# Performance work log

Hardware: AMD Instinct MI355X
Metric: run time of the kernel (lower is better)

Reference implementation:

```python
import jax, jax.numpy as jnp
import numpy as np

B, FEAT, SPD_H, CTRL_H, N_CMD = 32768, 512, 128, 256, 4


def _p(key, shape, fan_in):
    # torch nn.Linear default init: U(-1/sqrt(fan_in), 1/sqrt(fan_in))
    lim = 1.0 / np.sqrt(fan_in)
    return jax.random.uniform(key, shape, jnp.float32, -lim, lim)


def setup_inputs() -> dict:
    key = jax.random.key(0)
    ks = iter(jax.random.split(key, 32))
    inp = {
        "feat": jax.random.normal(next(ks), (B, FEAT), jnp.float32),
        "speed": jax.random.uniform(next(ks), (B,), jnp.float32),
        "command": jax.random.randint(next(ks), (B,), 0, N_CMD, jnp.int32),
        "ms_w1": _p(next(ks), (1, SPD_H), 1), "ms_b1": _p(next(ks), (SPD_H,), 1),
        "ms_w2": _p(next(ks), (SPD_H, SPD_H), SPD_H), "ms_b2": _p(next(ks), (SPD_H,), SPD_H),
        "ms_w3": _p(next(ks), (SPD_H, SPD_H), SPD_H), "ms_b3": _p(next(ks), (SPD_H,), SPD_H),
        # speed_pred_module: 512 -> 256 -> 256 -> 1
        "sp_w1": _p(next(ks), (FEAT, CTRL_H), FEAT), "sp_b1": _p(next(ks), (CTRL_H,), FEAT),
        "sp_w2": _p(next(ks), (CTRL_H, CTRL_H), CTRL_H), "sp_b2": _p(next(ks), (CTRL_H,), CTRL_H),
        "sp_w3": _p(next(ks), (CTRL_H, 1), CTRL_H), "sp_b3": _p(next(ks), (1,), CTRL_H),
        # join_module: Linear(640, 512)
        "join_w": _p(next(ks), (FEAT + SPD_H, FEAT), FEAT + SPD_H),
        "join_b": _p(next(ks), (FEAT,), FEAT + SPD_H),
        # 4 control heads: 512 -> 256 -> 256 -> 3 (stacked on expert axis e)
        "ctrl_w1": _p(next(ks), (N_CMD, FEAT, CTRL_H), FEAT), "ctrl_b1": _p(next(ks), (N_CMD, CTRL_H), FEAT),
        "ctrl_w2": _p(next(ks), (N_CMD, CTRL_H, CTRL_H), CTRL_H), "ctrl_b2": _p(next(ks), (N_CMD, CTRL_H), CTRL_H),
        "ctrl_w3": _p(next(ks), (N_CMD, CTRL_H, 3), CTRL_H), "ctrl_b3": _p(next(ks), (N_CMD, 3), CTRL_H),
    }
    return inp


def _mlp(x, w1, b1, w2, b2, w3, b3):
    # FullyConnectedNet: Linear, ReLU, Linear, Dropout(p=0 -> noop), ReLU, Linear
    h = jax.nn.relu(x @ w1 + b1)
    h = jax.nn.relu(h @ w2 + b2)
    return h @ w3 + b3


def reference(feat, speed, command,
              ms_w1, ms_b1, ms_w2, ms_b2, ms_w3, ms_b3,
              sp_w1, sp_b1, sp_w2, sp_b2, sp_w3, sp_b3,
              join_w, join_b,
              ctrl_w1, ctrl_b1, ctrl_w2, ctrl_b2, ctrl_w3, ctrl_b3):
    v = _mlp(speed[:, None], ms_w1, ms_b1, ms_w2, ms_b2, ms_w3, ms_b3)      # [B,128]
    joined = jnp.concatenate([feat, v], axis=1) @ join_w + join_b           # [B,512]
    v_p = _mlp(feat, sp_w1, sp_b1, sp_w2, sp_b2, sp_w3, sp_b3)              # [B,1]
    # command-indexed dispatch: compute all 4 heads densely, then select per sample
    h1 = jax.nn.relu(jnp.einsum('bd,edh->beh', joined, ctrl_w1) + ctrl_b1)  # [B,4,256]
    h2 = jax.nn.relu(jnp.einsum('beh,ehk->bek', h1, ctrl_w2) + ctrl_b2)     # [B,4,256]
    act_all = jnp.einsum('bek,eko->beo', h2, ctrl_w3) + ctrl_b3             # [B,4,3]
    action = jnp.take_along_axis(act_all, command[:, None, None].astype(jnp.int32), axis=1)[:, 0]  # [B,3]
    throttle = jax.nn.sigmoid(action[:, 0])
    steering = jnp.tanh(action[:, 1])
    brake = jax.nn.sigmoid(action[:, 2])
    return v_p, throttle, brake, steering
```

## Files before the change

kernel.cpp:

```cpp
#include <hip/hip_runtime.h>
#include <hip/hip_bf16.h>
#include <stdint.h>
#include <math.h>

#define BB 32768
#define FEAT 512
#define SPD_H 128
#define CTRL_H 256
#define NCMD 4

typedef __attribute__((ext_vector_type(8))) short bf16x8;
typedef __attribute__((ext_vector_type(4))) float f32x4;

__device__ __forceinline__ unsigned short f2bf(float f) {
  union { float f; uint32_t u; } v; v.f = f;
  uint32_t u = v.u;
  return (unsigned short)((u + 0x7fffu + ((u >> 16) & 1u)) >> 16);
}

__device__ __forceinline__ void async16(const unsigned short* g, unsigned short* l) {
  __builtin_amdgcn_global_load_lds(
      (const __attribute__((address_space(1))) unsigned int*)g,
      (__attribute__((address_space(3))) unsigned int*)l, 16, 0, 0);
}

__device__ __forceinline__ void gemm128(
    const unsigned short* __restrict__ A, int lda,
    const int* __restrict__ perm, int m_start, int m_cnt,
    const unsigned short* __restrict__ W, const float* __restrict__ bi,
    unsigned short* __restrict__ C, int ldc, int relu, int K, int mt, int nt) {
  extern __shared__ __align__(16) unsigned char dynsm[];
  unsigned short* As = (unsigned short*)dynsm;
  unsigned short* Bs = As + 128 * 32;

  const int m0 = mt * 128;
  if (m0 >= m_cnt) return;
  const int n0 = nt * 128;
  const int t = threadIdx.x;
  const int w = t >> 6, lane = t & 63;
  const int wm = w & 1, wn = w >> 1;

  f32x4 acc[4][4];
#pragma unroll
  for (int i = 0; i < 4; ++i)
#pragma unroll
    for (int j = 0; j < 4; ++j)
#pragma unroll
      for (int r = 0; r < 4; ++r) acc[i][j][r] = 0.f;

  const int fr = lane & 15;
  const int fk = (lane >> 4) * 8;

  const unsigned short* agp[2]; const unsigned short* bgp[2];
  unsigned short* al[2]; unsigned short* bl[2];
#pragma unroll
  for (int it = 0; it < 2; ++it) {
    int row = w * 32 + it * 16 + (lane >> 2);
    int seg8 = (lane & 3) * 8;
    int rl = m0 + row;
    if (rl >= m_cnt) rl = m_cnt - 1;
    int grow = perm ? perm[m_start + rl] : (m_start + rl);
    agp[it] = A + (size_t)grow * lda + seg8;
    bgp[it] = W + (size_t)(n0 + row) * K + seg8;
    al[it] = As + (w * 32 + it * 16) * 32;
    bl[it] = Bs + (w * 32 + it * 16) * 32;
  }

  for (int k0 = 0; k0 < K; k0 += 32) {
#pragma unroll
    for (int it = 0; it < 2; ++it) {
      async16(agp[it] + k0, al[it]);
      async16(bgp[it] + k0, bl[it]);
    }
    __syncthreads();
    bf16x8 af[4], bfv[4];
#pragma unroll
    for (int i = 0; i < 4; ++i)
      af[i] = *(const bf16x8*)(As + (wm * 64 + i * 16 + fr) * 32 + fk);
#pragma unroll
    for (int j = 0; j < 4; ++j)
      bfv[j] = *(const bf16x8*)(Bs + (wn * 64 + j * 16 + fr) * 32 + fk);
#pragma unroll
    for (int i = 0; i < 4; ++i)
#pragma unroll
      for (int j = 0; j < 4; ++j)
        acc[i][j] = __builtin_amdgcn_mfma_f32_16x16x32_bf16(af[i], bfv[j], acc[i][j], 0, 0, 0);
    __syncthreads();
  }

  const int rquad = (lane >> 4) * 4;
  const int cidx = lane & 15;

  float bv[4];
#pragma unroll
  for (int j = 0; j < 4; ++j) bv[j] = bi ? bi[n0 + wn * 64 + j * 16 + cidx] : 0.f;

  unsigned short (*bscr)[136] = (unsigned short(*)[136])dynsm;
#pragma unroll
  for (int c = 0; c < 4; ++c) {
    if (wm == (c >> 1)) {
#pragma unroll
      for (int j = 0; j < 4; ++j) {
#pragma unroll
        for (int ii = 0; ii < 2; ++ii) {
          int i = 2 * (c & 1) + ii;
          int lr = ii * 16 + rquad;
#pragma unroll
          for (int r = 0; r < 4; ++r) {
            float v = acc[i][j][r] + bv[j];
            if (relu) v = fmaxf(v, 0.f);
            bscr[lr + r][wn * 64 + j * 16 + cidx] = f2bf(v);
          }
        }
      }
    }
    __syncthreads();
#pragma unroll
    for (int q = 0; q < 2; ++q) {
      int sg = t + 256 * q;
      int lr = sg >> 4, cs = (sg & 15) * 8;
      int grow = m0 + c * 32 + lr;
      if (grow < m_cnt)
        *(bf16x8*)(C + (size_t)(m_start + grow) * ldc + (n0 + cs)) =
            *(const bf16x8*)(&bscr[lr][cs]);
    }
    __syncthreads();
  }
}

struct WSeg { const float* src; unsigned short* dst; int K; int N; int ldd; };
struct PrepArgs {
  WSeg s[12];
  int start[13];
  const float* join_w; unsigned short* wjbf;
  const float* feat; unsigned short* ajoin;
  const int* cmd; int* wavecnt;
  const float* join_b; const float* ctrl_w1; const float* ctrl_b1; float* b_f;
};
__launch_bounds__(256)
__global__ void k_prep(PrepArgs a) {
  int bx = blockIdx.x, t = threadIdx.x;
  if (bx < 16384) {
    int idx = bx * 256 + t;
    int i = idx >> 7;
    int j4 = (idx & 127) << 2;
    float4 f = *(const float4*)(a.feat + (size_t)i * FEAT + j4);
    ushort4 o;
    o.x = f2bf(f.x); o.y = f2bf(f.y); o.z = f2bf(f.z); o.w = f2bf(f.w);
    *(ushort4*)(a.ajoin + (size_t)i * 640 + j4) = o;
    return;
  }
  int rel = bx - 16384;
  if (rel < 320) {
    int idx = rel * 256 + t;
    float4 f = *(const float4*)(a.join_w + (size_t)idx * 4);
    ushort4 o;
    o.x = f2bf(f.x); o.y = f2bf(f.y); o.z = f2bf(f.z); o.w = f2bf(f.w);
    *(ushort4*)(a.wjbf + (size_t)idx * 4) = o;
    return;
  }
  rel -= 320;
  if (rel < a.start[12]) {
    __shared__ float tb[32][33];
    int si = 0;
    while (rel >= a.start[si + 1]) ++si;
    WSeg sg = a.s[si];
    int tile = rel - a.start[si];
    int tkx = sg.K >> 5;
    int tn = tile / tkx;
    int tk = tile - tn * tkx;
    int k0 = tk * 32, n0 = tn * 32;
    int tx = t & 31, ty = t >> 5;
#pragma unroll
    for (int j = 0; j < 4; ++j)
      tb[ty + j * 8][tx] = sg.src[(size_t)(k0 + ty + j * 8) * sg.N + n0 + tx];
    __syncthreads();
#pragma unroll
    for (int j = 0; j < 4; ++j)
      sg.dst[(size_t)(n0 + ty + j * 8) * sg.ldd + k0 + tx] = f2bf(tb[tx][ty + j * 8]);
    return;
  }
  rel -= a.start[12];
  if (rel < 128) {
    int i = rel * 256 + t;
    int c = a.cmd[i];
    int wid = i >> 6;
    int lane = t & 63;
#pragma unroll
    for (int cv = 0; cv < NCMD; ++cv) {
      unsigned long long m = __ballot(c == cv);
      if (lane == 0) a.wavecnt[cv * 512 + wid] = __popcll(m);
    }
    return;
  }
  int e = rel - 128;
  float s0 = a.ctrl_b1[e * 256 + t], s1 = 0.f, s2 = 0.f, s3 = 0.f;
  const float* w = a.ctrl_w1 + (size_t)e * 512 * 256 + t;
#pragma unroll 4
  for (int m = 0; m < 512; m += 4) {
    s0 = fmaf(a.join_b[m + 0], w[(size_t)(m + 0) * 256], s0);
    s1 = fmaf(a.join_b[m + 1], w[(size_t)(m + 1) * 256], s1);
    s2 = fmaf(a.join_b[m + 2], w[(size_t)(m + 2) * 256], s2);
    s3 = fmaf(a.join_b[m + 3], w[(size_t)(m + 3) * 256], s3);
  }
  a.b_f[e * 256 + t] = (s0 + s1) + (s2 + s3);
}

struct MidArgs {
  const int* cmd; const int* wavecnt; int* perm; int* offs;
  const unsigned short* c_w1t; const unsigned short* wjbf; unsigned short* wf_t;
  const float* speed;
  const float* ms_w1; const float* ms_b1;
  const unsigned short* ms_w2t; const float* ms_b2;
  const unsigned short* ms_w3t; const float* ms_b3;
  unsigned short* ajoin;
  int* tile_e; int* tile_r0; int* ntl;
};
__launch_bounds__(256)
__global__ void k_mid(MidArgs a) {
  int b = blockIdx.x, t = threadIdx.x;
  if (b >= 168) {
    extern __shared__ __align__(16) unsigned char dynsm[];
    unsigned short (*hw)[136] = (unsigned short(*)[136])dynsm;
    unsigned short* BsM = (unsigned short*)(dynsm + 128 * 136 * 2);
    const int m0 = (b - 168) * 128;
    const int w = t >> 6, lane = t & 63;
    const int wm = w & 1, wn = w >> 1;
    const int fr = lane & 15, fk = (lane >> 4) * 8;
    const int rquad = (lane >> 4) * 4, cidx = lane & 15;
    {
      int r = t >> 1, half = t & 1;
      float s = a.speed[m0 + r];
#pragma unroll
      for (int c0 = 0; c0 < 64; c0 += 4) {
        int c = half * 64 + c0;
        float4 wv = *(const float4*)(a.ms_w1 + c);
        float4 bv = *(const float4*)(a.ms_b1 + c);
        hw[r][c + 0] = f2bf(fmaxf(fmaf(s, wv.x, bv.x), 0.f));
        hw[r][c + 1] = f2bf(fmaxf(fmaf(s, wv.y, bv.y), 0.f));
        hw[r][c + 2] = f2bf(fmaxf(fmaf(s, wv.z, bv.z), 0.f));
        hw[r][c + 3] = f2bf(fmaxf(fmaf(s, wv.w, bv.w), 0.f));
      }
    }
    __syncthreads();
    for (int layer = 0; layer < 2; ++layer) {
      const unsigned short* Wt = layer ? a.ms_w3t : a.ms_w2t;
      const float* bb = layer ? a.ms_b3 : a.ms_b2;
      f32x4 acc[4][4];
#pragma unroll
      for (int i = 0; i < 4; ++i)
#pragma unroll
        for (int j = 0; j < 4; ++j)
#pragma unroll
          for (int r = 0; r < 4; ++r) acc[i][j][r] = 0.f;
      for (int k0 = 0; k0 < 128; k0 += 32) {
#pragma unroll
        for (int it = 0; it < 2; ++it) {
          int row = w * 32 + it * 16 + (lane >> 2);
          async16(Wt + (size_t)row * 128 + k0 + (lane & 3) * 8,
                  BsM + (w * 32 + it * 16) * 32);
        }
        __syncthreads();
        bf16x8 af[4], bfv[4];
#pragma unroll
        for (int i = 0; i < 4; ++i)
          af[i] = *(const bf16x8*)(&hw[wm * 64 + i * 16 + fr][k0 + fk]);
#pragma unroll
        for (int j = 0; j < 4; ++j)
          bfv[j] = *(const bf16x8*)(BsM + (wn * 64 + j * 16 + fr) * 32 + fk);
#pragma unroll
        for (int i = 0; i < 4; ++i)
#pragma unroll
          for (int j = 0; j < 4; ++j)
            acc[i][j] = __builtin_amdgcn_mfma_f32_16x16x32_bf16(af[i], bfv[j], acc[i][j], 0, 0, 0);
        __syncthreads();
      }
#pragma unroll
      for (int j = 0; j < 4; ++j) {
        int col = wn * 64 + j * 16 + cidx;
        float bv = bb[col];
#pragma unroll
        for (int i = 0; i < 4; ++i) {
          int row = wm * 64 + i * 16 + rquad;
#pragma unroll
          for (int r = 0; r < 4; ++r) {
            float v = acc[i][j][r] + bv;
            if (layer == 0) v = fmaxf(v, 0.f);
            hw[row + r][col] = f2bf(v);
          }
        }
      }
      __syncthreads();
    }
    {
      int r = t >> 1, half = t & 1;
#pragma unroll
      for (int c8 = 0; c8 < 8; ++c8)
        *(bf16x8*)(a.ajoin + (size_t)(m0 + r) * 640 + 512 + half * 64 + c8 * 8) =
            *(const bf16x8*)(&hw[r][half * 64 + c8 * 8]);
    }
    return;
  }
  if (b >= 128) {
    int idx = b - 128;
    int mt = idx & 7, nt = idx >> 3;
    gemm128(a.c_w1t, 512, nullptr, 0, 1024, a.wjbf, nullptr, a.wf_t, 640, 0, 512, mt, nt);
    return;
  }
  __shared__ int pf[NCMD][4];
  __shared__ int tot[NCMD];
  int c = t >> 6, lane = t & 63;
  int v[8]; int s = 0;
#pragma unroll
  for (int q = 0; q < 8; ++q) { v[q] = a.wavecnt[c * 512 + lane * 8 + q]; s += v[q]; }
  int p = s;
#pragma unroll
  for (int m = 1; m < 64; m <<= 1) { int o = __shfl_up(p, m, 64); if (lane >= m) p += o; }
  int excl = p - s;
  if (lane == 63) tot[c] = p;
  if (lane == ((4 * b) >> 3)) {
    int base_off = (4 * b) & 7;
    int run = excl;
#pragma unroll
    for (int q = 0; q < 8; ++q) {
      if (q >= base_off && q < base_off + 4) pf[c][q - base_off] = run;
      run += v[q];
    }
  }
  __syncthreads();
  int soffs[NCMD + 1];
  soffs[0] = 0;
#pragma unroll
  for (int e = 0; e < NCMD; ++e) soffs[e + 1] = soffs[e] + tot[e];
  if (b == 0 && t == 0)
    for (int e = 0; e <= NCMD; ++e) a.offs[e] = soffs[e];
  int i = b * 256 + t;
  int mc = a.cmd[i];
  int lwid = t >> 6;
  int rank = 0, base = 0;
#pragma unroll
  for (int cv = 0; cv < NCMD; ++cv) {
    unsigned long long m = __ballot(mc == cv);
    if (mc == cv) {
      rank = __popcll(m & ((1ull << lane) - 1ull));
      base = soffs[cv] + pf[cv][lwid];
    }
  }
  a.perm[base + rank] = i;

  if (b == 0) {
    int toff[NCMD + 1];
    toff[0] = 0;
#pragma unroll
    for (int ee = 0; ee < NCMD; ++ee) toff[ee + 1] = toff[ee] + ((tot[ee] + 63) >> 6);
    if (t == 0) a.ntl[0] = toff[NCMD];
    for (int ti = t; ti < toff[NCMD]; ti += 256) {
      int ee = 0;
      while (ti >= toff[ee + 1]) ++ee;
      a.tile_e[ti] = ee;
      a.tile_r0[ti] = soffs[ee] + (ti - toff[ee]) * 64;
    }
  }
}

struct TailArgs {
  const unsigned short* ajoin;
  const unsigned short* wf_t;  const float* b_f;
  const unsigned short* sp_w1t; const float* sp_b1;
  const unsigned short* c_w2t; const float* ctrl_b2;
  const unsigned short* sp_w2t; const float* sp_b2;
  const float* ctrl_w3; const float* ctrl_b3;
  const float* sp_w3; const float* sp_b3;
  const int* perm; const int* seg;
  const int* tile_e; const int* tile_r0; const int* ntl;
  float* out;
};
__launch_bounds__(256, 3)
__global__ void k_tail(TailArgs a) {
  extern __shared__ __align__(16) unsigned char dynsm[];
  unsigned short* As = (unsigned short*)dynsm;
  unsigned short* h1 = (unsigned short*)(dynsm + 16384);
  float* pscr = (float*)dynsm;

  const int t = threadIdx.x;
  const int w = t >> 6, lane = t & 63;
  const int fr = lane & 15, fcg = lane >> 4;
  const int rquad = fcg * 4, cidx = fr;
  const int fkS = ((fcg ^ (fr & 3)) << 3);

  int is_sp, e = 0, NC;
  const unsigned short *W1, *W2;
  const float *b1, *b2;
  int r0, rend;
  if (blockIdx.x < 512) {
    is_sp = 1; NC = 8;
    W1 = a.sp_w1t; W2 = a.sp_w2t; b1 = a.sp_b1; b2 = a.sp_b2;
    r0 = blockIdx.x * 64; rend = BB;
  } else {
    int ti = blockIdx.x - 512;
    if (ti >= a.ntl[0]) return;
    is_sp = 0; e = a.tile_e[ti]; NC = 10;
    W1 = a.wf_t + (size_t)e * 256 * 640;
    W2 = a.c_w2t + (size_t)e * 65536;
    b1 = a.b_f + e * 256; b2 = a.ctrl_b2 + e * 256;
    r0 = a.tile_r0[ti]; rend = a.seg[e + 1];
  }
  const int K = is_sp ? 512 : 640;

  const unsigned short* agp[2];
  {
    int rl = r0 + w * 16 + (lane >> 2);
    if (rl >= rend) rl = rend - 1;
    int grow = is_sp ? rl : a.perm[rl];
    const unsigned short* g0 =
        a.ajoin + (size_t)grow * 640 + (((lane & 3) ^ ((lane >> 2) & 3)) << 3);
    agp[0] = g0; agp[1] = g0 + 32;
  }
  unsigned short* alb0 = As + w * 16 * 32;
  unsigned short* alb1 = As + 2048 + w * 16 * 32;

  const unsigned short* bp[4];
#pragma unroll
  for (int j = 0; j < 4; ++j)
    bp[j] = W1 + (size_t)(w * 64 + j * 16 + fr) * K + fcg * 8;

  f32x4 acc[4][4];
#pragma unroll
  for (int i = 0; i < 4; ++i)
#pragma unroll
    for (int j = 0; j < 4; ++j)
#pragma unroll
      for (int r = 0; r < 4; ++r) acc[i][j][r] = 0.f;

  async16(agp[0], alb0);
  async16(agp[1], alb1);

  for (int c = 0; c < NC; ++c) {
    const int cur = (c & 1) * 4096;
    if (c + 1 < NC) {
      const int nb = ((c + 1) & 1) * 4096;
      async16(agp[0] + (c + 1) * 64, alb0 + nb);
      async16(agp[1] + (c + 1) * 64, alb1 + nb);
      asm volatile("s_waitcnt vmcnt(2)" ::: "memory");
    } else {
      asm volatile("s_waitcnt vmcnt(0)" ::: "memory");
    }
    __builtin_amdgcn_s_barrier();
#pragma unroll
    for (int ks = 0; ks < 2; ++ks) {
      const int k0 = c * 64 + ks * 32;
      bf16x8 af[4], bv[4];
#pragma unroll
      for (int i = 0; i < 4; ++i)
        af[i] = *(const bf16x8*)(As + cur + ks * 2048 + (i * 16 + fr) * 32 + fkS);
#pragma unroll
      for (int j = 0; j < 4; ++j)
        bv[j] = *(const bf16x8*)(bp[j] + k0);
#pragma unroll
      for (int i = 0; i < 4; ++i)
#pragma unroll
        for (int j = 0; j < 4; ++j)
          acc[i][j] = __builtin_amdgcn_mfma_f32_16x16x32_bf16(af[i], bv[j], acc[i][j], 0, 0, 0);
    }
    __builtin_amdgcn_s_barrier();
  }

#pragma unroll
  for (int j = 0; j < 4; ++j) {
    const int col = w * 64 + j * 16 + cidx;
    const float bj = b1[col];
    const int c8 = col >> 3, cl = col & 7;
#pragma unroll
    for (int i = 0; i < 4; ++i) {
#pragma unroll
      for (int r = 0; r < 4; ++r) {
        const int row = i * 16 + rquad + r;
        h1[(row << 8) + (((c8 ^ (row & 7)) << 3) | cl)] =
            f2bf(fmaxf(acc[i][j][r] + bj, 0.f));
      }
    }
  }
  __syncthreads();

  const unsigned short* bp2[4];
#pragma unroll
  for (int j = 0; j < 4; ++j)
    bp2[j] = W2 + (size_t)(w * 64 + j * 16 + fr) * 256 + fcg * 8;

#pragma unroll
  for (int i = 0; i < 4; ++i)
#pragma unroll
    for (int j = 0; j < 4; ++j)
#pragma unroll
      for (int r = 0; r < 4; ++r) acc[i][j][r] = 0.f;

#pragma unroll 2
  for (int k0 = 0; k0 < 256; k0 += 32) {
    bf16x8 af[4], bv[4];
#pragma unroll
    for (int i = 0; i < 4; ++i) {
      const int row = i * 16 + fr;
      const int c8 = (k0 >> 3) + fcg;
      af[i] = *(const bf16x8*)(h1 + (row << 8) + ((c8 ^ (row & 7)) << 3));
    }
#pragma unroll
    for (int j = 0; j < 4; ++j)
      bv[j] = *(const bf16x8*)(bp2[j] + k0);
#pragma unroll
    for (int i = 0; i < 4; ++i)
#pragma unroll
      for (int j = 0; j < 4; ++j)
        acc[i][j] = __builtin_amdgcn_mfma_f32_16x16x32_bf16(af[i], bv[j], acc[i][j], 0, 0, 0);
  }

  float b2v[4], w30[4], w31[4], w32[4];
#pragma unroll
  for (int j = 0; j < 4; ++j) {
    const int col = w * 64 + j * 16 + cidx;
    b2v[j] = b2[col];
    if (is_sp) {
      w30[j] = a.sp_w3[col]; w31[j] = 0.f; w32[j] = 0.f;
    } else {
      const float* wp = a.ctrl_w3 + (size_t)e * 768 + col * 3;
      w30[j] = wp[0]; w31[j] = wp[1]; w32[j] = wp[2];
    }
  }
#pragma unroll
  for (int i = 0; i < 4; ++i) {
#pragma unroll
    for (int r = 0; r < 4; ++r) {
      float s0 = 0.f, s1 = 0.f, s2 = 0.f;
#pragma unroll
      for (int j = 0; j < 4; ++j) {
        const float v = fmaxf(acc[i][j][r] + b2v[j], 0.f);
        s0 = fmaf(v, w30[j], s0);
        if (!is_sp) { s1 = fmaf(v, w31[j], s1); s2 = fmaf(v, w32[j], s2); }
      }
#pragma unroll
      for (int m = 1; m <= 8; m <<= 1) {
        s0 += __shfl_xor(s0, m, 64);
        if (!is_sp) { s1 += __shfl_xor(s1, m, 64); s2 += __shfl_xor(s2, m, 64); }
      }
      if (cidx == 0) {
        const int row = i * 16 + rquad + r;
        pscr[(row * 4 + w) * 3 + 0] = s0;
        if (!is_sp) {
          pscr[(row * 4 + w) * 3 + 1] = s1;
          pscr[(row * 4 + w) * 3 + 2] = s2;
        }
      }
    }
  }
  __syncthreads();

  if (is_sp) {
    if (t < 64) {
      float s = pscr[t * 12] + pscr[t * 12 + 3] + pscr[t * 12 + 6] + pscr[t * 12 + 9]
              + a.sp_b3[0];
      a.out[r0 + t] = s;
    }
  } else {
    if (t < 192) {
      const int row = t / 3, o = t - row * 3;
      const int rl = r0 + row;
      if (rl < rend) {
        float s = pscr[row * 12 + o] + pscr[row * 12 + 3 + o] +
                  pscr[row * 12 + 6 + o] + pscr[row * 12 + 9 + o] +
                  a.ctrl_b3[e * 3 + o];
        const int orig = a.perm[rl];
        if (o == 0)      a.out[BB + orig]     = 1.f / (1.f + __expf(-s));
        else if (o == 2) a.out[2 * BB + orig] = 1.f / (1.f + __expf(-s));
        else             a.out[3 * BB + orig] = tanhf(s);
      }
    }
  }
}

static inline size_t align256(size_t x) { return (x + 255) & ~(size_t)255; }

extern "C" void kernel_launch(void* const* d_in, const int* in_sizes, int n_in,
                              void* d_out, int out_size, void* d_ws, size_t ws_size,
                              hipStream_t stream) {
  const float* feat   = (const float*)d_in[0];
  const float* speed  = (const float*)d_in[1];
  const int*   command= (const int*)d_in[2];
  const float* ms_w1  = (const float*)d_in[3];
  const float* ms_b1  = (const float*)d_in[4];
  const float* ms_w2  = (const float*)d_in[5];
  const float* ms_b2  = (const float*)d_in[6];
  const float* ms_w3  = (const float*)d_in[7];
  const float* ms_b3  = (const float*)d_in[8];
  const float* sp_w1  = (const float*)d_in[9];
  const float* sp_b1  = (const float*)d_in[10];
  const float* sp_w2  = (const float*)d_in[11];
  const float* sp_b2  = (const float*)d_in[12];
  const float* sp_w3  = (const float*)d_in[13];
  const float* sp_b3  = (const float*)d_in[14];
  const float* join_w = (const float*)d_in[15];
  const float* join_b = (const float*)d_in[16];
  const float* ctrl_w1= (const float*)d_in[17];
  const float* ctrl_b1= (const float*)d_in[18];
  const float* ctrl_w2= (const float*)d_in[19];
  const float* ctrl_b2= (const float*)d_in[20];
  const float* ctrl_w3= (const float*)d_in[21];
  const float* ctrl_b3= (const float*)d_in[22];
  float* out = (float*)d_out;

  char* ws = (char*)d_ws;
  size_t off = 0;
  auto alloc = [&](size_t bytes) -> char* { char* p = ws + off; off = align256(off + bytes); return p; };

  unsigned short* ajoin  = (unsigned short*)alloc((size_t)BB * 640 * 2);
  unsigned short* wtp    = (unsigned short*)alloc(1998848ull * 2);
  int* perm    = (int*)alloc((size_t)BB * 4);
  int* cnt     = (int*)alloc(64);
  int* wavecnt = (int*)alloc(4 * 512 * 4);
  float* b_f   = (float*)alloc(4 * 256 * 4);
  int* tile_e  = (int*)alloc(520 * 4);
  int* tile_r0 = (int*)alloc(520 * 4);
  int* ntl     = (int*)alloc(64);

  unsigned short* sp_w1t = wtp;
  unsigned short* sp_w2t = wtp + 131072;
  unsigned short* ms_w2t = wtp + 196608;
  unsigned short* ms_w3t = wtp + 212992;
  unsigned short* c_w1t  = wtp + 229376;
  unsigned short* c_w2t  = wtp + 753664;
  unsigned short* wjbf   = wtp + 1015808;
  unsigned short* wf_t   = wtp + 1343488;

  PrepArgs P;
  P.s[0] = { sp_w1, sp_w1t, 512, 256, 512 };
  P.s[1] = { sp_w2, sp_w2t, 256, 256, 256 };
  P.s[2] = { ms_w2, ms_w2t, 128, 128, 128 };
  P.s[3] = { ms_w3, ms_w3t, 128, 128, 128 };
  for (int e = 0; e < 4; ++e) P.s[4 + e] = { ctrl_w1 + (size_t)e * 512 * 256, c_w1t + (size_t)e * 131072, 512, 256, 512 };
  for (int e = 0; e < 4; ++e) P.s[8 + e] = { ctrl_w2 + (size_t)e * 256 * 256, c_w2t + (size_t)e * 65536, 256, 256, 256 };
  P.start[0] = 0;
  for (int i = 0; i < 12; ++i)
    P.start[i + 1] = P.start[i] + (P.s[i].K >> 5) * (P.s[i].N >> 5);
  P.join_w = join_w; P.wjbf = wjbf;
  P.feat = feat; P.ajoin = ajoin;
  P.cmd = command; P.wavecnt = wavecnt;
  P.join_b = join_b; P.ctrl_w1 = ctrl_w1; P.ctrl_b1 = ctrl_b1; P.b_f = b_f;
  int prep_blocks = 16384 + 320 + P.start[12] + 128 + 4;

  k_prep<<<prep_blocks, 256, 0, stream>>>(P);

  MidArgs Mi;
  Mi.cmd = command; Mi.wavecnt = wavecnt; Mi.perm = perm; Mi.offs = cnt + 4;
  Mi.c_w1t = c_w1t; Mi.wjbf = wjbf; Mi.wf_t = wf_t;
  Mi.speed = speed;
  Mi.ms_w1 = ms_w1; Mi.ms_b1 = ms_b1;
  Mi.ms_w2t = ms_w2t; Mi.ms_b2 = ms_b2;
  Mi.ms_w3t = ms_w3t; Mi.ms_b3 = ms_b3;
  Mi.ajoin = ajoin;
  Mi.tile_e = tile_e; Mi.tile_r0 = tile_r0; Mi.ntl = ntl;
  k_mid<<<168 + 256, 256, 128 * 136 * 2 + 128 * 32 * 2, stream>>>(Mi);

  TailArgs T;
  T.ajoin = ajoin; T.wf_t = wf_t; T.b_f = b_f;
  T.sp_w1t = sp_w1t; T.sp_b1 = sp_b1;
  T.c_w2t = c_w2t; T.ctrl_b2 = ctrl_b2;
  T.sp_w2t = sp_w2t; T.sp_b2 = sp_b2;
  T.ctrl_w3 = ctrl_w3; T.ctrl_b3 = ctrl_b3;
  T.sp_w3 = sp_w3; T.sp_b3 = sp_b3;
  T.perm = perm; T.seg = cnt + 4;
  T.tile_e = tile_e; T.tile_r0 = tile_r0; T.ntl = ntl;
  T.out = out;
  k_tail<<<dim3(512 + 516), 256, 49152, stream>>>(T);
}
```

Measured before the change: 240.7 us.

## Fuse feat bf16 conversion into tail GEMM loads and halve row tiles

Removes the separate pass that converts feat to bf16 into a 640-wide joined buffer. The tail kernel now reads fp32 feat directly, packs it to bf16 in registers, and writes it into a swizzled LDS tile. The speed-MLP output goes to its own 128-wide buffer instead of the joined one. Row tiles shrink from 64 to 32, which doubles the block count and raises the occupancy hint to 4. In exchange, async global-to-LDS loads become register staging with two barriers per K-chunk, and weight reads are amortized over fewer rows.

Measured after the change: 267.8 us. 1.11x slower.

```diff
diff --git a/kernel.cpp b/kernel.cpp
--- a/kernel.cpp
+++ b/kernel.cpp
@@ -16,6 +16,15 @@
   union { float f; uint32_t u; } v; v.f = f;
   uint32_t u = v.u;
   return (unsigned short)((u + 0x7fffu + ((u >> 16) & 1u)) >> 16);
+}
+
+__device__ __forceinline__ bf16x8 pack8(float4 a, float4 b) {
+  bf16x8 r;
+  r[0] = (short)f2bf(a.x); r[1] = (short)f2bf(a.y);
+  r[2] = (short)f2bf(a.z); r[3] = (short)f2bf(a.w);
+  r[4] = (short)f2bf(b.x); r[5] = (short)f2bf(b.y);
+  r[6] = (short)f2bf(b.z); r[7] = (short)f2bf(b.w);
+  return r;
 }
 
 __device__ __forceinline__ void async16(const unsigned short* g, unsigned short* l) {
@@ -133,33 +142,21 @@
   WSeg s[12];
   int start[13];
   const float* join_w; unsigned short* wjbf;
-  const float* feat; unsigned short* ajoin;
   const int* cmd; int* wavecnt;
   const float* join_b; const float* ctrl_w1; const float* ctrl_b1; float* b_f;
 };
 __launch_bounds__(256)
 __global__ void k_prep(PrepArgs a) {
   int bx = blockIdx.x, t = threadIdx.x;
-  if (bx < 16384) {
+  if (bx < 320) {
     int idx = bx * 256 + t;
-    int i = idx >> 7;
-    int j4 = (idx & 127) << 2;
-    float4 f = *(const float4*)(a.feat + (size_t)i * FEAT + j4);
-    ushort4 o;
-    o.x = f2bf(f.x); o.y = f2bf(f.y); o.z = f2bf(f.z); o.w = f2bf(f.w);
-    *(ushort4*)(a.ajoin + (size_t)i * 640 + j4) = o;
-    return;
-  }
-  int rel = bx - 16384;
-  if (rel < 320) {
-    int idx = rel * 256 + t;
     float4 f = *(const float4*)(a.join_w + (size_t)idx * 4);
     ushort4 o;
     o.x = f2bf(f.x); o.y = f2bf(f.y); o.z = f2bf(f.z); o.w = f2bf(f.w);
     *(ushort4*)(a.wjbf + (size_t)idx * 4) = o;
     return;
   }
-  rel -= 320;
+  int rel = bx - 320;
   if (rel < a.start[12]) {
     __shared__ float tb[32][33];
     int si = 0;
@@ -213,7 +210,7 @@
   const float* ms_w1; const float* ms_b1;
   const unsigned short* ms_w2t; const float* ms_b2;
   const unsigned short* ms_w3t; const float* ms_b3;
-  unsigned short* ajoin;
+  unsigned short* msout;
   int* tile_e; int* tile_r0; int* ntl;
 };
 __launch_bounds__(256)
@@ -296,7 +293,7 @@
       int r = t >> 1, half = t & 1;
 #pragma unroll
       for (int c8 = 0; c8 < 8; ++c8)
-        *(bf16x8*)(a.ajoin + (size_t)(m0 + r) * 640 + 512 + half * 64 + c8 * 8) =
+        *(bf16x8*)(a.msout + (size_t)(m0 + r) * 128 + half * 64 + c8 * 8) =
             *(const bf16x8*)(&hw[r][half * 64 + c8 * 8]);
     }
     return;
@@ -352,19 +349,20 @@
     int toff[NCMD + 1];
     toff[0] = 0;
 #pragma unroll
-    for (int ee = 0; ee < NCMD; ++ee) toff[ee + 1] = toff[ee] + ((tot[ee] + 63) >> 6);
+    for (int ee = 0; ee < NCMD; ++ee) toff[ee + 1] = toff[ee] + ((tot[ee] + 31) >> 5);
     if (t == 0) a.ntl[0] = toff[NCMD];
     for (int ti = t; ti < toff[NCMD]; ti += 256) {
       int ee = 0;
       while (ti >= toff[ee + 1]) ++ee;
       a.tile_e[ti] = ee;
-      a.tile_r0[ti] = soffs[ee] + (ti - toff[ee]) * 64;
+      a.tile_r0[ti] = soffs[ee] + (ti - toff[ee]) * 32;
     }
   }
 }
 
 struct TailArgs {
-  const unsigned short* ajoin;
+  const float* feat;
+  const unsigned short* msout;
   const unsigned short* wf_t;  const float* b_f;
   const unsigned short* sp_w1t; const float* sp_b1;
   const unsigned short* c_w2t; const float* ctrl_b2;
@@ -375,29 +373,29 @@
   const int* tile_e; const int* tile_r0; const int* ntl;
   float* out;
 };
-__launch_bounds__(256, 3)
+__launch_bounds__(256, 4)
 __global__ void k_tail(TailArgs a) {
   extern __shared__ __align__(16) unsigned char dynsm[];
   unsigned short* As = (unsigned short*)dynsm;
-  unsigned short* h1 = (unsigned short*)(dynsm + 16384);
+  unsigned short* h1 = (unsigned short*)(dynsm + 8192);
   float* pscr = (float*)dynsm;
 
   const int t = threadIdx.x;
   const int w = t >> 6, lane = t & 63;
   const int fr = lane & 15, fcg = lane >> 4;
   const int rquad = fcg * 4, cidx = fr;
-  const int fkS = ((fcg ^ (fr & 3)) << 3);
+  const int row_s = t >> 3, cg = t & 7;
 
   int is_sp, e = 0, NC;
   const unsigned short *W1, *W2;
   const float *b1, *b2;
   int r0, rend;
-  if (blockIdx.x < 512) {
+  if (blockIdx.x < 1024) {
     is_sp = 1; NC = 8;
     W1 = a.sp_w1t; W2 = a.sp_w2t; b1 = a.sp_b1; b2 = a.sp_b2;
-    r0 = blockIdx.x * 64; rend = BB;
+    r0 = blockIdx.x * 32; rend = BB;
   } else {
-    int ti = blockIdx.x - 512;
+    int ti = blockIdx.x - 1024;
     if (ti >= a.ntl[0]) return;
     is_sp = 0; e = a.tile_e[ti]; NC = 10;
     W1 = a.wf_t + (size_t)e * 256 * 640;
@@ -407,62 +405,74 @@
   }
   const int K = is_sp ? 512 : 640;
 
-  const unsigned short* agp[2];
+  const float* fsrc; const unsigned short* msrc;
   {
-    int rl = r0 + w * 16 + (lane >> 2);
+    int rl = r0 + row_s;
     if (rl >= rend) rl = rend - 1;
     int grow = is_sp ? rl : a.perm[rl];
-    const unsigned short* g0 =
-        a.ajoin + (size_t)grow * 640 + (((lane & 3) ^ ((lane >> 2) & 3)) << 3);
-    agp[0] = g0; agp[1] = g0 + 32;
-  }
-  unsigned short* alb0 = As + w * 16 * 32;
-  unsigned short* alb1 = As + 2048 + w * 16 * 32;
+    fsrc = a.feat + (size_t)grow * 512 + cg * 8;
+    msrc = a.msout + (size_t)grow * 128 + cg * 8;
+  }
+  unsigned short* wslot = As + row_s * 64 + ((cg ^ (row_s & 7)) << 3);
 
   const unsigned short* bp[4];
 #pragma unroll
   for (int j = 0; j < 4; ++j)
     bp[j] = W1 + (size_t)(w * 64 + j * 16 + fr) * K + fcg * 8;
 
-  f32x4 acc[4][4];
-#pragma unroll
-  for (int i = 0; i < 4; ++i)
+  f32x4 acc[2][4];
+#pragma unroll
+  for (int i = 0; i < 2; ++i)
 #pragma unroll
     for (int j = 0; j < 4; ++j)
 #pragma unroll
       for (int r = 0; r < 4; ++r) acc[i][j][r] = 0.f;
 
-  async16(agp[0], alb0);
-  async16(agp[1], alb1);
+  {
+    float4 fa = *(const float4*)(fsrc);
+    float4 fb = *(const float4*)(fsrc + 4);
+    *(bf16x8*)(wslot) = pack8(fa, fb);
+  }
+  __syncthreads();
 
   for (int c = 0; c < NC; ++c) {
-    const int cur = (c & 1) * 4096;
-    if (c + 1 < NC) {
-      const int nb = ((c + 1) & 1) * 4096;
-      async16(agp[0] + (c + 1) * 64, alb0 + nb);
-      async16(agp[1] + (c + 1) * 64, alb1 + nb);
-      asm volatile("s_waitcnt vmcnt(2)" ::: "memory");
-    } else {
-      asm volatile("s_waitcnt vmcnt(0)" ::: "memory");
-    }
-    __builtin_amdgcn_s_barrier();
+    float4 fa, fb; bf16x8 mreg;
+    const int k0n = (c + 1) * 64;
+    const bool pre = (c + 1 < NC);
+    if (pre) {
+      if (k0n < 512) {
+        fa = *(const float4*)(fsrc + k0n);
+        fb = *(const float4*)(fsrc + k0n + 4);
+      } else {
+        mreg = *(const bf16x8*)(msrc + (k0n - 512));
+      }
+    }
+    const unsigned short* cbuf = As + (c & 1) * 2048;
 #pragma unroll
     for (int ks = 0; ks < 2; ++ks) {
       const int k0 = c * 64 + ks * 32;
-      bf16x8 af[4], bv[4];
-#pragma unroll
-      for (int i = 0; i < 4; ++i)
-        af[i] = *(const bf16x8*)(As + cur + ks * 2048 + (i * 16 + fr) * 32 + fkS);
+      bf16x8 af[2], bv[4];
+#pragma unroll
+      for (int i = 0; i < 2; ++i)
+        af[i] = *(const bf16x8*)(cbuf + (i * 16 + fr) * 64 +
+                                 (((ks * 4 + fcg) ^ (fr & 7)) << 3));
 #pragma unroll
       for (int j = 0; j < 4; ++j)
         bv[j] = *(const bf16x8*)(bp[j] + k0);
 #pragma unroll
-      for (int i = 0; i < 4; ++i)
+      for (int i = 0; i < 2; ++i)
 #pragma unroll
         for (int j = 0; j < 4; ++j)
           acc[i][j] = __builtin_amdgcn_mfma_f32_16x16x32_bf16(af[i], bv[j], acc[i][j], 0, 0, 0);
     }
-    __builtin_amdgcn_s_barrier();
+    __syncthreads();
+    if (pre) {
+      bf16x8 pk;
+      if (k0n < 512) pk = pack8(fa, fb);
+      else pk = mreg;
+      *(bf16x8*)(wslot + ((c + 1) & 1) * 2048) = pk;
+    }
+    __syncthreads();
   }
 
 #pragma unroll
@@ -471,7 +481,7 @@
     const float bj = b1[col];
     const int c8 = col >> 3, cl = col & 7;
 #pragma unroll
-    for (int i = 0; i < 4; ++i) {
+    for (int i = 0; i < 2; ++i) {
 #pragma unroll
       for (int r = 0; r < 4; ++r) {
         const int row = i * 16 + rquad + r;
@@ -488,7 +498,7 @@
     bp2[j] = W2 + (size_t)(w * 64 + j * 16 + fr) * 256 + fcg * 8;
 
 #pragma unroll
-  for (int i = 0; i < 4; ++i)
+  for (int i = 0; i < 2; ++i)
 #pragma unroll
     for (int j = 0; j < 4; ++j)
 #pragma unroll
@@ -496,9 +506,9 @@
 
 #pragma unroll 2
   for (int k0 = 0; k0 < 256; k0 += 32) {
-    bf16x8 af[4], bv[4];
-#pragma unroll
-    for (int i = 0; i < 4; ++i) {
+    bf16x8 af[2], bv[4];
+#pragma unroll
+    for (int i = 0; i < 2; ++i) {
       const int row = i * 16 + fr;
       const int c8 = (k0 >> 3) + fcg;
       af[i] = *(const bf16x8*)(h1 + (row << 8) + ((c8 ^ (row & 7)) << 3));
@@ -507,7 +517,7 @@
     for (int j = 0; j < 4; ++j)
       bv[j] = *(const bf16x8*)(bp2[j] + k0);
 #pragma unroll
-    for (int i = 0; i < 4; ++i)
+    for (int i = 0; i < 2; ++i)
 #pragma unroll
       for (int j = 0; j < 4; ++j)
         acc[i][j] = __builtin_amdgcn_mfma_f32_16x16x32_bf16(af[i], bv[j], acc[i][j], 0, 0, 0);
@@ -526,7 +536,7 @@
     }
   }
 #pragma unroll
-  for (int i = 0; i < 4; ++i) {
+  for (int i = 0; i < 2; ++i) {
 #pragma unroll
     for (int r = 0; r < 4; ++r) {
       float s0 = 0.f, s1 = 0.f, s2 = 0.f;
@@ -554,13 +564,13 @@
   __syncthreads();
 
   if (is_sp) {
-    if (t < 64) {
+    if (t < 32) {
       float s = pscr[t * 12] + pscr[t * 12 + 3] + pscr[t * 12 + 6] + pscr[t * 12 + 9]
               + a.sp_b3[0];
       a.out[r0 + t] = s;
     }
   } else {
-    if (t < 192) {
+    if (t < 96) {
       const int row = t / 3, o = t - row * 3;
       const int rl = r0 + row;
       if (rl < rend) {
@@ -610,14 +620,14 @@
   size_t off = 0;
   auto alloc = [&](size_t bytes) -> char* { char* p = ws + off; off = align256(off + bytes); return p; };
 
-  unsigned short* ajoin  = (unsigned short*)alloc((size_t)BB * 640 * 2);
+  unsigned short* msout  = (unsigned short*)alloc((size_t)BB * 128 * 2);
   unsigned short* wtp    = (unsigned short*)alloc(1998848ull * 2);
   int* perm    = (int*)alloc((size_t)BB * 4);
   int* cnt     = (int*)alloc(64);
   int* wavecnt = (int*)alloc(4 * 512 * 4);
   float* b_f   = (float*)alloc(4 * 256 * 4);
-  int* tile_e  = (int*)alloc(520 * 4);
-  int* tile_r0 = (int*)alloc(520 * 4);
+  int* tile_e  = (int*)alloc(1056 * 4);
+  int* tile_r0 = (int*)alloc(1056 * 4);
   int* ntl     = (int*)alloc(64);
 
   unsigned short* sp_w1t = wtp;
@@ -640,10 +650,9 @@
   for (int i = 0; i < 12; ++i)
     P.start[i + 1] = P.start[i] + (P.s[i].K >> 5) * (P.s[i].N >> 5);
   P.join_w = join_w; P.wjbf = wjbf;
-  P.feat = feat; P.ajoin = ajoin;
   P.cmd = command; P.wavecnt = wavecnt;
   P.join_b = join_b; P.ctrl_w1 = ctrl_w1; P.ctrl_b1 = ctrl_b1; P.b_f = b_f;
-  int prep_blocks = 16384 + 320 + P.start[12] + 128 + 4;
+  int prep_blocks = 320 + P.start[12] + 128 + 4;
 
   k_prep<<<prep_blocks, 256, 0, stream>>>(P);
 
@@ -654,12 +663,13 @@
   Mi.ms_w1 = ms_w1; Mi.ms_b1 = ms_b1;
   Mi.ms_w2t = ms_w2t; Mi.ms_b2 = ms_b2;
   Mi.ms_w3t = ms_w3t; Mi.ms_b3 = ms_b3;
-  Mi.ajoin = ajoin;
+  Mi.msout = msout;
   Mi.tile_e = tile_e; Mi.tile_r0 = tile_r0; Mi.ntl = ntl;
   k_mid<<<168 + 256, 256, 128 * 136 * 2 + 128 * 32 * 2, stream>>>(Mi);
 
   TailArgs T;
-  T.ajoin = ajoin; T.wf_t = wf_t; T.b_f = b_f;
+  T.feat = feat; T.msout = msout;
+  T.wf_t = wf_t; T.b_f = b_f;
   T.sp_w1t = sp_w1t; T.sp_b1 = sp_b1;
   T.c_w2t = c_w2t; T.ctrl_b2 = ctrl_b2;
   T.sp_w2t = sp_w2t; T.sp_b2 = sp_b2;
@@ -668,5 +678,5 @@
   T.perm = perm; T.seg = cnt + 4;
   T.tile_e = tile_e; T.tile_r0 = tile_r0; T.ntl = ntl;
   T.out = out;
-  k_tail<<<dim3(512 + 516), 256, 49152, stream>>>(T);
-}
+  k_tail<<<dim3(1024 + 1028), 256, 24576, stream>>>(T);
+}
```

## Fuse feat fp32-to-bf16 conversion into tail GEMM A-tile loads

Applied to the files above, without the earlier changes.

Drops the separate prep pass that converted feat to bf16 into a 640-wide joined buffer. The tail kernel now reads fp32 feat rows directly (through perm for the expert heads), converts them to bf16 in registers, and writes a swizzled 64-wide K tile into LDS. The speed-MLP output goes to its own narrow bf16 buffer. The async global-to-LDS copies become register-staged double buffering. This removes the large write and re-read of the intermediate, but the tail now reads twice as many bytes for feat and uses more registers. The expert heads and the speed-prediction path each re-read feat, so feat is fetched in fp32 more than once.

Result: faster. 230.0 us (-4.5%).

```diff
diff --git a/kernel.cpp b/kernel.cpp
--- a/kernel.cpp
+++ b/kernel.cpp
@@ -16,6 +16,15 @@
   union { float f; uint32_t u; } v; v.f = f;
   uint32_t u = v.u;
   return (unsigned short)((u + 0x7fffu + ((u >> 16) & 1u)) >> 16);
+}
+
+__device__ __forceinline__ bf16x8 pack8(float4 a, float4 b) {
+  bf16x8 r;
+  r[0] = (short)f2bf(a.x); r[1] = (short)f2bf(a.y);
+  r[2] = (short)f2bf(a.z); r[3] = (short)f2bf(a.w);
+  r[4] = (short)f2bf(b.x); r[5] = (short)f2bf(b.y);
+  r[6] = (short)f2bf(b.z); r[7] = (short)f2bf(b.w);
+  return r;
 }
 
 __device__ __forceinline__ void async16(const unsigned short* g, unsigned short* l) {
@@ -133,33 +142,21 @@
   WSeg s[12];
   int start[13];
   const float* join_w; unsigned short* wjbf;
-  const float* feat; unsigned short* ajoin;
   const int* cmd; int* wavecnt;
   const float* join_b; const float* ctrl_w1; const float* ctrl_b1; float* b_f;
 };
 __launch_bounds__(256)
 __global__ void k_prep(PrepArgs a) {
   int bx = blockIdx.x, t = threadIdx.x;
-  if (bx < 16384) {
+  if (bx < 320) {
     int idx = bx * 256 + t;
-    int i = idx >> 7;
-    int j4 = (idx & 127) << 2;
-    float4 f = *(const float4*)(a.feat + (size_t)i * FEAT + j4);
-    ushort4 o;
-    o.x = f2bf(f.x); o.y = f2bf(f.y); o.z = f2bf(f.z); o.w = f2bf(f.w);
-    *(ushort4*)(a.ajoin + (size_t)i * 640 + j4) = o;
-    return;
-  }
-  int rel = bx - 16384;
-  if (rel < 320) {
-    int idx = rel * 256 + t;
     float4 f = *(const float4*)(a.join_w + (size_t)idx * 4);
     ushort4 o;
     o.x = f2bf(f.x); o.y = f2bf(f.y); o.z = f2bf(f.z); o.w = f2bf(f.w);
     *(ushort4*)(a.wjbf + (size_t)idx * 4) = o;
     return;
   }
-  rel -= 320;
+  int rel = bx - 320;
   if (rel < a.start[12]) {
     __shared__ float tb[32][33];
     int si = 0;
@@ -213,7 +210,7 @@
   const float* ms_w1; const float* ms_b1;
   const unsigned short* ms_w2t; const float* ms_b2;
   const unsigned short* ms_w3t; const float* ms_b3;
-  unsigned short* ajoin;
+  unsigned short* msout;
   int* tile_e; int* tile_r0; int* ntl;
 };
 __launch_bounds__(256)
@@ -296,7 +293,7 @@
       int r = t >> 1, half = t & 1;
 #pragma unroll
       for (int c8 = 0; c8 < 8; ++c8)
-        *(bf16x8*)(a.ajoin + (size_t)(m0 + r) * 640 + 512 + half * 64 + c8 * 8) =
+        *(bf16x8*)(a.msout + (size_t)(m0 + r) * 128 + half * 64 + c8 * 8) =
             *(const bf16x8*)(&hw[r][half * 64 + c8 * 8]);
     }
     return;
@@ -364,7 +361,8 @@
 }
 
 struct TailArgs {
-  const unsigned short* ajoin;
+  const float* feat;
+  const unsigned short* msout;
   const unsigned short* wf_t;  const float* b_f;
   const unsigned short* sp_w1t; const float* sp_b1;
   const unsigned short* c_w2t; const float* ctrl_b2;
@@ -386,7 +384,7 @@
   const int w = t >> 6, lane = t & 63;
   const int fr = lane & 15, fcg = lane >> 4;
   const int rquad = fcg * 4, cidx = fr;
-  const int fkS = ((fcg ^ (fr & 3)) << 3);
+  const int row_s = t >> 2, sl = t & 3;
 
   int is_sp, e = 0, NC;
   const unsigned short *W1, *W2;
@@ -407,17 +405,17 @@
   }
   const int K = is_sp ? 512 : 640;
 
-  const unsigned short* agp[2];
+  const float* fsrc; const unsigned short* msrc;
   {
-    int rl = r0 + w * 16 + (lane >> 2);
+    int rl = r0 + row_s;
     if (rl >= rend) rl = rend - 1;
     int grow = is_sp ? rl : a.perm[rl];
-    const unsigned short* g0 =
-        a.ajoin + (size_t)grow * 640 + (((lane & 3) ^ ((lane >> 2) & 3)) << 3);
-    agp[0] = g0; agp[1] = g0 + 32;
-  }
-  unsigned short* alb0 = As + w * 16 * 32;
-  unsigned short* alb1 = As + 2048 + w * 16 * 32;
+    fsrc = a.feat + (size_t)grow * 512 + sl * 16;
+    msrc = a.msout + (size_t)grow * 128 + sl * 16;
+  }
+  const int xr = row_s & 7;
+  unsigned short* wp0 = As + row_s * 64 + (((2 * sl) ^ xr) << 3);
+  unsigned short* wp1 = As + row_s * 64 + (((2 * sl + 1) ^ xr) << 3);
 
   const unsigned short* bp[4];
 #pragma unroll
@@ -432,27 +430,47 @@
 #pragma unroll
       for (int r = 0; r < 4; ++r) acc[i][j][r] = 0.f;
 
-  async16(agp[0], alb0);
-  async16(agp[1], alb1);
+  float4 g0, g1, g2, g3; bf16x8 mv0, mv1;
+
+#define LOADA(cc)                                                        \
+  do {                                                                   \
+    if ((cc) < 8) {                                                      \
+      g0 = *(const float4*)(fsrc + (cc) * 64 + 0);                       \
+      g1 = *(const float4*)(fsrc + (cc) * 64 + 4);                       \
+      g2 = *(const float4*)(fsrc + (cc) * 64 + 8);                       \
+      g3 = *(const float4*)(fsrc + (cc) * 64 + 12);                      \
+    } else {                                                             \
+      mv0 = *(const bf16x8*)(msrc + ((cc) - 8) * 64 + 0);                \
+      mv1 = *(const bf16x8*)(msrc + ((cc) - 8) * 64 + 8);                \
+    }                                                                    \
+  } while (0)
+
+#define WRITEA(cc, bufb)                                                 \
+  do {                                                                   \
+    bf16x8 s0_, s1_;                                                     \
+    if ((cc) < 8) { s0_ = pack8(g0, g1); s1_ = pack8(g2, g3); }          \
+    else { s0_ = mv0; s1_ = mv1; }                                       \
+    *(bf16x8*)(wp0 + (bufb)) = s0_;                                      \
+    *(bf16x8*)(wp1 + (bufb)) = s1_;                                      \
+  } while (0)
+
+  LOADA(0);
+  WRITEA(0, 0);
+  LOADA(1);
+  __syncthreads();
 
   for (int c = 0; c < NC; ++c) {
-    const int cur = (c & 1) * 4096;
-    if (c + 1 < NC) {
-      const int nb = ((c + 1) & 1) * 4096;
-      async16(agp[0] + (c + 1) * 64, alb0 + nb);
-      async16(agp[1] + (c + 1) * 64, alb1 + nb);
-      asm volatile("s_waitcnt vmcnt(2)" ::: "memory");
-    } else {
-      asm volatile("s_waitcnt vmcnt(0)" ::: "memory");
-    }
-    __builtin_amdgcn_s_barrier();
+    const int cr = (c & 1) * 4096;
+    if (c + 1 < NC) WRITEA(c + 1, ((c + 1) & 1) * 4096);
+    if (c + 2 < NC) LOADA(c + 2);
 #pragma unroll
     for (int ks = 0; ks < 2; ++ks) {
       const int k0 = c * 64 + ks * 32;
       bf16x8 af[4], bv[4];
 #pragma unroll
       for (int i = 0; i < 4; ++i)
-        af[i] = *(const bf16x8*)(As + cur + ks * 2048 + (i * 16 + fr) * 32 + fkS);
+        af[i] = *(const bf16x8*)(As + cr + (i * 16 + fr) * 64 +
+                                 (((ks * 4 + fcg) ^ (fr & 7)) << 3));
 #pragma unroll
       for (int j = 0; j < 4; ++j)
         bv[j] = *(const bf16x8*)(bp[j] + k0);
@@ -462,8 +480,10 @@
         for (int j = 0; j < 4; ++j)
           acc[i][j] = __builtin_amdgcn_mfma_f32_16x16x32_bf16(af[i], bv[j], acc[i][j], 0, 0, 0);
     }
-    __builtin_amdgcn_s_barrier();
-  }
+    __syncthreads();
+  }
+#undef LOADA
+#undef WRITEA
 
 #pragma unroll
   for (int j = 0; j < 4; ++j) {
@@ -610,14 +630,14 @@
   size_t off = 0;
   auto alloc = [&](size_t bytes) -> char* { char* p = ws + off; off = align256(off + bytes); return p; };
 
-  unsigned short* ajoin  = (unsigned short*)alloc((size_t)BB * 640 * 2);
+  unsigned short* msout  = (unsigned short*)alloc((size_t)BB * 128 * 2);
   unsigned short* wtp    = (unsigned short*)alloc(1998848ull * 2);
   int* perm    = (int*)alloc((size_t)BB * 4);
   int* cnt     = (int*)alloc(64);
   int* wavecnt = (int*)alloc(4 * 512 * 4);
   float* b_f   = (float*)alloc(4 * 256 * 4);
-  int* tile_e  = (int*)alloc(520 * 4);
-  int* tile_r0 = (int*)alloc(520 * 4);
+  int* tile_e  = (int*)alloc(1056 * 4);
+  int* tile_r0 = (int*)alloc(1056 * 4);
   int* ntl     = (int*)alloc(64);
 
   unsigned short* sp_w1t = wtp;
@@ -640,10 +660,9 @@
   for (int i = 0; i < 12; ++i)
     P.start[i + 1] = P.start[i] + (P.s[i].K >> 5) * (P.s[i].N >> 5);
   P.join_w = join_w; P.wjbf = wjbf;
-  P.feat = feat; P.ajoin = ajoin;
   P.cmd = command; P.wavecnt = wavecnt;
   P.join_b = join_b; P.ctrl_w1 = ctrl_w1; P.ctrl_b1 = ctrl_b1; P.b_f = b_f;
-  int prep_blocks = 16384 + 320 + P.start[12] + 128 + 4;
+  int prep_blocks = 320 + P.start[12] + 128 + 4;
 
   k_prep<<<prep_blocks, 256, 0, stream>>>(P);
 
@@ -654,12 +673,13 @@
   Mi.ms_w1 = ms_w1; Mi.ms_b1 = ms_b1;
   Mi.ms_w2t = ms_w2t; Mi.ms_b2 = ms_b2;
   Mi.ms_w3t = ms_w3t; Mi.ms_b3 = ms_b3;
-  Mi.ajoin = ajoin;
+  Mi.msout = msout;
   Mi.tile_e = tile_e; Mi.tile_r0 = tile_r0; Mi.ntl = ntl;
   k_mid<<<168 + 256, 256, 128 * 136 * 2 + 128 * 32 * 2, stream>>>(Mi);
 
   TailArgs T;
-  T.ajoin = ajoin; T.wf_t = wf_t; T.b_f = b_f;
+  T.feat = feat; T.msout = msout;
+  T.wf_t = wf_t; T.b_f = b_f;
   T.sp_w1t = sp_w1t; T.sp_b1 = sp_b1;
   T.c_w2t = c_w2t; T.ctrl_b2 = ctrl_b2;
   T.sp_w2t = sp_w2t; T.sp_b2 = sp_b2;
```
